# Kernel optimization log

Hardware: AMD Instinct MI355X
Metric: run time of the kernel (lower is better)

## Reference

```python
import jax, jax.numpy as jnp
import numpy as np


def setup_inputs() -> dict:
    key = jax.random.key(0)
    B, DP, N = 4, 3, 8192
    positions = jax.random.normal(key, (B, DP, N), dtype=jnp.float32)
    return {"positions": positions, "k": 16}


def reference(positions, k):
    # positions: [B, Dp, N] ('simple' data_format)
    # Pairwise squared Euclidean distances between all N points per batch:
    # d2[b, i, j] = ||x_i - x_j||^2 = ||x_i||^2 + ||x_j||^2 - 2 x_i . x_j
    sq = jnp.sum(positions * positions, axis=1)                     # [B, N]
    dots = jnp.einsum('bdn,bdm->bnm', positions, positions)         # [B, N, N]
    d2 = sq[:, :, None] + sq[:, None, :] - 2.0 * dots               # [B, N, N]
    # k nearest neighbors (smallest distance; includes self at distance ~0)
    neg_d, idx = jax.lax.top_k(-d2, k)                              # [B, N, K]
    # Layer transposes raw op output [B, N, K] -> [B, K, N]
    NN = jnp.transpose(idx, (0, 2, 1)).astype(jnp.int32)            # [B, K, N]
    distances = jnp.transpose(-neg_d, (0, 2, 1))                    # [B, K, N]
    return (NN, distances)
```

## Files before the change

kernel.cpp:

```cpp
#include <hip/hip_runtime.h>
#include <stdint.h>

#define NPTS 8192
#define NPAIR 4096
#define NB 4
#define KNN 16
#define RQ 2
#define CCAP 24
#define DCAP 256
#define MARGIN 1.5e-3f

typedef unsigned long long u64;
typedef unsigned int u32;
typedef unsigned short u16;
typedef float f32x2 __attribute__((ext_vector_type(2)));

__device__ __forceinline__ u32 f2ord(float f) {
    u32 b = __float_as_uint(f);
    return (b & 0x80000000u) ? ~b : (b | 0x80000000u);
}
__device__ __forceinline__ float ord2f(u32 u) {
    u32 b = (u & 0x80000000u) ? (u & 0x7fffffffu) : ~u;
    return __uint_as_float(b);
}
__device__ __forceinline__ u64 shflx64(u64 v, int m) {
    u32 lo = (u32)v, hi = (u32)(v >> 32);
    lo = __shfl_xor(lo, m, 64);
    hi = __shfl_xor(hi, m, 64);
    return ((u64)hi << 32) | lo;
}

__global__ __launch_bounds__(256) void pack_kernel(const float* __restrict__ pos,
                                                   float4* __restrict__ pos8) {
    int t = blockIdx.x * 256 + threadIdx.x;
    int b = t >> 12;
    int m = t & (NPAIR - 1);
    const float* p = pos + (size_t)b * 3 * NPTS;
    float2 x = *(const float2*)&p[2 * m];
    float2 y = *(const float2*)&p[NPTS + 2 * m];
    float2 z = *(const float2*)&p[2 * NPTS + 2 * m];
    float s0 = __fadd_rn(__fadd_rn(__fmul_rn(x.x, x.x), __fmul_rn(y.x, y.x)), __fmul_rn(z.x, z.x));
    float s1 = __fadd_rn(__fadd_rn(__fmul_rn(x.y, x.y), __fmul_rn(y.y, y.y)), __fmul_rn(z.y, z.y));
    pos8[2 * t]     = make_float4(x.x, x.y, y.x, y.y);
    pos8[2 * t + 1] = make_float4(z.x, z.y, s0, s1);
}

#define RECOMP(r, idx, d2out)                                                           \
    { int _m = (int)(idx) >> 1, _h = (int)(idx) & 1;                                    \
      float4 _a = P8[2 * _m], _c = P8[2 * _m + 1];                                      \
      float _px = _h ? _a.y : _a.x, _py = _h ? _a.w : _a.z;                             \
      float _pz = _h ? _c.y : _c.x, _pw = _h ? _c.w : _c.z;                             \
      float _dot = __fmaf_rn(qz[r], _pz, __fmaf_rn(qy[r], _py, __fmul_rn(qx[r], _px))); \
      d2out = __fsub_rn(__fadd_rn(qw[r], _pw), __fmul_rn(2.0f, _dot)); }

__global__ __launch_bounds__(256) void knn_kernel(const float4* __restrict__ pos8,
                                                  float* __restrict__ out) {
    __shared__ u16 col[4][RQ][CCAP][64];
    __shared__ u16 dense[4][RQ][DCAP];
    const int lane = threadIdx.x & 63;
    const int wv = threadIdx.x >> 6;
    const int rowbase = blockIdx.x * (4 * RQ) + wv * RQ;
    const int b = rowbase >> 13;
    const int ib = rowbase & (NPTS - 1);
    const float4* __restrict__ P8 = pos8 + (size_t)b * NPAIR * 2;
    const u64 below = (1ull << lane) - 1ull;

    float qx[RQ], qy[RQ], qz[RQ], qw[RQ];
    {
        int m = ib >> 1;
        float4 a = P8[2 * m], cc = P8[2 * m + 1];
        qx[0] = a.x; qy[0] = a.z; qz[0] = cc.x; qw[0] = cc.z;
        qx[1] = a.y; qy[1] = a.w; qz[1] = cc.y; qw[1] = cc.w;
    }
    f32x2 qxv[RQ], qyv[RQ], qzv[RQ];
#pragma unroll
    for (int r = 0; r < RQ; ++r) {
        qxv[r] = (f32x2){qx[r], qx[r]};
        qyv[r] = (f32x2){qy[r], qy[r]};
        qzv[r] = (f32x2){qz[r], qz[r]};
    }
    const f32x2 n2v = {-2.0f, -2.0f};

    float Tm[RQ];
    int c[RQ];

    auto tighten = [&](int r) {
        u32 mn = 0xFFFFFFFFu;
#pragma unroll
        for (int t = 0; t < CCAP; ++t) {
            if (t < c[r]) {
                u32 idx = (u32)col[wv][r][t][lane];
                float d2; RECOMP(r, idx, d2);
                u32 o = f2ord(d2);
                mn = o < mn ? o : mn;
            }
        }
        u32 v = mn;
#pragma unroll
        for (int k = 2; k <= 64; k <<= 1)
#pragma unroll
            for (int j = k >> 1; j >= 1; j >>= 1) {
                u32 o = (u32)__shfl_xor((int)v, j, 64);
                bool up = ((lane & k) == 0) == ((lane & j) == 0);
                v = (up ? (v < o) : (v > o)) ? v : o;
            }
        u32 ordK = (u32)__shfl((int)v, 15, 64);
        int nc = 0;
#pragma unroll
        for (int t = 0; t < CCAP; ++t) {
            if (t < c[r]) {
                u32 idx = (u32)col[wv][r][t][lane];
                float d2; RECOMP(r, idx, d2);
                if (f2ord(d2) <= ordK) { col[wv][r][nc][lane] = (u16)idx; ++nc; }
            }
        }
        c[r] = nc;
#pragma unroll 1
        for (int it = 0; it < CCAP - 16; ++it) {
            if (c[r] > 16) {
                u64 mx = 0; int mt = 0;
#pragma unroll
                for (int t = 0; t < CCAP; ++t) {
                    if (t < c[r]) {
                        u32 idx = (u32)col[wv][r][t][lane];
                        float d2; RECOMP(r, idx, d2);
                        u64 key = ((u64)f2ord(d2) << 13) | idx;
                        if (key > mx) { mx = key; mt = t; }
                    }
                }
                col[wv][r][mt][lane] = col[wv][r][c[r] - 1][lane];
                c[r] -= 1;
            }
        }
        Tm[r] = (ord2f(ordK) - qw[r]) + MARGIN;
    };

#pragma unroll
    for (int s = 0; s < 4; ++s) {
        int m = s * 64 + lane;
#pragma unroll
        for (int r = 0; r < RQ; ++r) {
            col[wv][r][2 * s][lane]     = (u16)(2 * m);
            col[wv][r][2 * s + 1][lane] = (u16)(2 * m + 1);
        }
    }
    c[0] = 8; c[1] = 8;
    tighten(0); tighten(1);

#pragma unroll 1
    for (int g = 1; g < 16; ++g) {
        if (__ballot(c[0] >= CCAP - 8)) tighten(0);
        if (__ballot(c[1] >= CCAP - 8)) tighten(1);
        int base = g * 256;
        float4 A[4], C[4];
#pragma unroll
        for (int s = 0; s < 4; ++s) {
            int m = base + s * 64 + lane;
            A[s] = P8[2 * m];
            C[s] = P8[2 * m + 1];
        }
#pragma unroll
        for (int s = 0; s < 4; ++s) {
            int m = base + s * 64 + lane;
            f32x2 x01 = {A[s].x, A[s].y}, y01 = {A[s].z, A[s].w};
            f32x2 z01 = {C[s].x, C[s].y}, sq01 = {C[s].z, C[s].w};
#pragma unroll
            for (int r = 0; r < RQ; ++r) {
                f32x2 dot01 = __builtin_elementwise_fma(
                    qzv[r], z01, __builtin_elementwise_fma(qyv[r], y01, qxv[r] * x01));
                f32x2 val01 = __builtin_elementwise_fma(n2v, dot01, sq01);
                if (val01.x < Tm[r]) { col[wv][r][c[r]][lane] = (u16)(2 * m);     c[r]++; }
                if (val01.y < Tm[r]) { col[wv][r][c[r]][lane] = (u16)(2 * m + 1); c[r]++; }
            }
        }
    }

#pragma unroll
    for (int r = 0; r < RQ; ++r) {
        int sum = c[r];
#pragma unroll
        for (int s2 = 1; s2 < 64; s2 <<= 1) sum += __shfl_xor(sum, s2, 64);
        if (sum > 64) tighten(r);
        int nc = 0;
#pragma unroll 1
        for (int t = 0; t < CCAP; ++t) {
            bool valid = t < c[r];
            u64 bal = __ballot(valid);
            if (!bal) break;
            if (valid) dense[wv][r][nc + (int)__popcll(bal & below)] = col[wv][r][t][lane];
            nc += (int)__popcll(bal);
        }
        u64 myk = ~0ULL;
        if (nc <= 64) {
            bool valid = lane < nc;
            u32 idx = valid ? (u32)dense[wv][r][lane] : 0u;
            float d2; RECOMP(r, idx, d2);
            u64 v = valid ? (((u64)f2ord(d2) << 13) | idx) : ~0ULL;
#pragma unroll
            for (int k = 2; k <= 64; k <<= 1)
#pragma unroll
                for (int j = k >> 1; j >= 1; j >>= 1) {
                    u64 o = shflx64(v, j);
                    bool up = ((lane & k) == 0) == ((lane & j) == 0);
                    v = (up ? (v < o) : (v > o)) ? v : o;
                }
            myk = v;
        } else {
            u64 s4[4];
#pragma unroll
            for (int t = 0; t < 4; ++t) {
                int bi = t * 64 + lane;
                bool valid = bi < nc;
                u32 idx = valid ? (u32)dense[wv][r][bi] : 0u;
                float d2; RECOMP(r, idx, d2);
                s4[t] = valid ? (((u64)f2ord(d2) << 13) | idx) : ~0ULL;
            }
#pragma unroll 1
            for (int rr = 0; rr < KNN; ++rr) {
                u64 lm = s4[0];
#pragma unroll
                for (int t = 1; t < 4; ++t) lm = s4[t] < lm ? s4[t] : lm;
                u64 mm = lm;
#pragma unroll
                for (int s2 = 1; s2 < 64; s2 <<= 1) { u64 o = shflx64(mm, s2); mm = o < mm ? o : mm; }
#pragma unroll
                for (int t = 0; t < 4; ++t) s4[t] = (s4[t] == mm) ? ~0ULL : s4[t];
                if (lane == rr) myk = mm;
            }
        }
        if (lane < KNN) {
            int iq = ib + r;
            size_t o1 = (size_t)(b * KNN + lane) * NPTS + iq;
            out[o1] = (float)(u32)(myk & (u64)(NPTS - 1));
            out[(size_t)NB * KNN * NPTS + o1] = ord2f((u32)(myk >> 13));
        }
    }
}

extern "C" void kernel_launch(void* const* d_in, const int* in_sizes, int n_in,
                              void* d_out, int out_size, void* d_ws, size_t ws_size,
                              hipStream_t stream) {
    const float* pos = (const float*)d_in[0];
    float* out = (float*)d_out;
    float4* pos8 = (float4*)d_ws;

    pack_kernel<<<dim3(NB * NPAIR / 256), dim3(256), 0, stream>>>(pos, pos8);
    knn_kernel<<<dim3(NB * NPTS / 8), dim3(256), 0, stream>>>(pos8, out);
}
```

Measured before the change: 201.4 us.

## Seed kNN threshold from per-lane minima with bitonic rank and tighten more often

The initial pruning threshold now comes from a wave-wide bitonic sort of per-lane minimum distances, taking the 16th smallest. This replaces loading 8 candidates per lane and running a full tighten. Each lane also keeps a running minimum, and every other group a cheap rank-16 threshold update runs. Tighten now fires at more than 16 candidates, mid-group as well, and the candidate capacity shrinks from 24 to 20 to cut LDS use. The goal is to prune more points early and avoid costly recompute-based tightening, at the cost of extra shuffle sorts and a risk of column overflow or a threshold that is too tight.

```diff
diff --git a/kernel.cpp b/kernel.cpp
--- a/kernel.cpp
+++ b/kernel.cpp
@@ -6,7 +6,7 @@
 #define NB 4
 #define KNN 16
 #define RQ 2
-#define CCAP 24
+#define CCAP 20
 #define DCAP 256
 #define MARGIN 1.5e-3f
 
@@ -53,6 +53,21 @@
       float _dot = __fmaf_rn(qz[r], _pz, __fmaf_rn(qy[r], _py, __fmul_rn(qx[r], _px))); \
       d2out = __fsub_rn(__fadd_rn(qw[r], _pw), __fmul_rn(2.0f, _dot)); }
 
+#define PROC(Av, Cv, mm)                                                                \
+    {                                                                                   \
+        f32x2 x01 = {(Av).x, (Av).y}, y01 = {(Av).z, (Av).w};                           \
+        f32x2 z01 = {(Cv).x, (Cv).y}, sq01 = {(Cv).z, (Cv).w};                          \
+        _Pragma("unroll")                                                               \
+        for (int r = 0; r < RQ; ++r) {                                                  \
+            f32x2 dot01 = __builtin_elementwise_fma(                                    \
+                qzv[r], z01, __builtin_elementwise_fma(qyv[r], y01, qxv[r] * x01));     \
+            f32x2 val01 = __builtin_elementwise_fma(n2v, dot01, sq01);                  \
+            lmU[r] = fminf(lmU[r], fminf(val01.x, val01.y));                            \
+            if (val01.x < Tm[r]) { col[wv][r][c[r]][lane] = (u16)(2 * (mm));     c[r]++; } \
+            if (val01.y < Tm[r]) { col[wv][r][c[r]][lane] = (u16)(2 * (mm) + 1); c[r]++; } \
+        }                                                                               \
+    }
+
 __global__ __launch_bounds__(256) void knn_kernel(const float4* __restrict__ pos8,
                                                   float* __restrict__ out) {
     __shared__ u16 col[4][RQ][CCAP][64];
@@ -82,7 +97,25 @@
     const f32x2 n2v = {-2.0f, -2.0f};
 
     float Tm[RQ];
+    float lmU[RQ];
     int c[RQ];
+
+    auto rank16f = [&](float v) -> float {
+#pragma unroll
+        for (int k = 2; k <= 64; k <<= 1)
+#pragma unroll
+            for (int j = k >> 1; j >= 1; j >>= 1) {
+                float o = __shfl_xor(v, j, 64);
+                bool up = ((lane & k) == 0) == ((lane & j) == 0);
+                v = (up ? (v < o) : (v > o)) ? v : o;
+            }
+        return __shfl(v, 15, 64);
+    };
+
+    auto cheapT = [&](int r) {
+        float V16 = rank16f(lmU[r]);
+        Tm[r] = fminf(Tm[r], V16 + 2.0f * MARGIN);
+    };
 
     auto tighten = [&](int r) {
         u32 mn = 0xFFFFFFFFu;
@@ -132,25 +165,44 @@
                 c[r] -= 1;
             }
         }
-        Tm[r] = (ord2f(ordK) - qw[r]) + MARGIN;
+        Tm[r] = fminf(Tm[r], (ord2f(ordK) - qw[r]) + MARGIN);
     };
 
-#pragma unroll
-    for (int s = 0; s < 4; ++s) {
-        int m = s * 64 + lane;
+    {
+        float4 A0 = P8[2 * (0 * 64 + lane)], C0 = P8[2 * (0 * 64 + lane) + 1];
+        float4 A1 = P8[2 * (1 * 64 + lane)], C1 = P8[2 * (1 * 64 + lane) + 1];
 #pragma unroll
         for (int r = 0; r < RQ; ++r) {
-            col[wv][r][2 * s][lane]     = (u16)(2 * m);
-            col[wv][r][2 * s + 1][lane] = (u16)(2 * m + 1);
-        }
-    }
-    c[0] = 8; c[1] = 8;
-    tighten(0); tighten(1);
+            f32x2 x0 = {A0.x, A0.y}, y0 = {A0.z, A0.w}, z0 = {C0.x, C0.y}, s0 = {C0.z, C0.w};
+            f32x2 x1 = {A1.x, A1.y}, y1 = {A1.z, A1.w}, z1 = {C1.x, C1.y}, s1 = {C1.z, C1.w};
+            f32x2 v0 = __builtin_elementwise_fma(
+                n2v, __builtin_elementwise_fma(qzv[r], z0,
+                     __builtin_elementwise_fma(qyv[r], y0, qxv[r] * x0)), s0);
+            f32x2 v1 = __builtin_elementwise_fma(
+                n2v, __builtin_elementwise_fma(qzv[r], z1,
+                     __builtin_elementwise_fma(qyv[r], y1, qxv[r] * x1)), s1);
+            float mn = fminf(fminf(v0.x, v0.y), fminf(v1.x, v1.y));
+            float V16 = rank16f(mn);
+            Tm[r] = V16 + 2.0f * MARGIN;
+            lmU[r] = mn;
+            c[r] = 0;
+            if (v0.x < Tm[r]) { col[wv][r][c[r]][lane] = (u16)(2 * lane);            c[r]++; }
+            if (v0.y < Tm[r]) { col[wv][r][c[r]][lane] = (u16)(2 * lane + 1);        c[r]++; }
+            if (v1.x < Tm[r]) { col[wv][r][c[r]][lane] = (u16)(2 * (64 + lane));     c[r]++; }
+            if (v1.y < Tm[r]) { col[wv][r][c[r]][lane] = (u16)(2 * (64 + lane) + 1); c[r]++; }
+        }
+    }
+    {
+        float4 A2 = P8[2 * (128 + lane)], C2 = P8[2 * (128 + lane) + 1];
+        float4 A3 = P8[2 * (192 + lane)], C3 = P8[2 * (192 + lane) + 1];
+        PROC(A2, C2, 128 + lane);
+        PROC(A3, C3, 192 + lane);
+    }
 
 #pragma unroll 1
     for (int g = 1; g < 16; ++g) {
-        if (__ballot(c[0] >= CCAP - 8)) tighten(0);
-        if (__ballot(c[1] >= CCAP - 8)) tighten(1);
+        if (__ballot(c[0] > 16)) tighten(0);
+        if (__ballot(c[1] > 16)) tighten(1);
         int base = g * 256;
         float4 A[4], C[4];
 #pragma unroll
@@ -159,20 +211,13 @@
             A[s] = P8[2 * m];
             C[s] = P8[2 * m + 1];
         }
-#pragma unroll
-        for (int s = 0; s < 4; ++s) {
-            int m = base + s * 64 + lane;
-            f32x2 x01 = {A[s].x, A[s].y}, y01 = {A[s].z, A[s].w};
-            f32x2 z01 = {C[s].x, C[s].y}, sq01 = {C[s].z, C[s].w};
-#pragma unroll
-            for (int r = 0; r < RQ; ++r) {
-                f32x2 dot01 = __builtin_elementwise_fma(
-                    qzv[r], z01, __builtin_elementwise_fma(qyv[r], y01, qxv[r] * x01));
-                f32x2 val01 = __builtin_elementwise_fma(n2v, dot01, sq01);
-                if (val01.x < Tm[r]) { col[wv][r][c[r]][lane] = (u16)(2 * m);     c[r]++; }
-                if (val01.y < Tm[r]) { col[wv][r][c[r]][lane] = (u16)(2 * m + 1); c[r]++; }
-            }
-        }
+        PROC(A[0], C[0], base + lane);
+        PROC(A[1], C[1], base + 64 + lane);
+        if (__ballot(c[0] > 16)) tighten(0);
+        if (__ballot(c[1] > 16)) tighten(1);
+        PROC(A[2], C[2], base + 128 + lane);
+        PROC(A[3], C[3], base + 192 + lane);
+        if ((g & 1) == 0) { cheapT(0); cheapT(1); }
     }
 
 #pragma unroll
```

Measured after the change: 274.4 us. +36.3%, slower.
